# Kernel optimization log

Measured on AMD Instinct MI355X. Metric: run time of the kernel, lower is better.

The kernel has to match this reference:

```python
import jax, jax.numpy as jnp
import numpy as np

S, D_MODEL, D_RNN = 256, 512, 512  # module's broadcasting requires d_rnn == d_model


def setup_inputs() -> dict:
    key = jax.random.key(0)
    k1, k2, k3, k4 = jax.random.split(key, 4)
    x = jax.random.normal(k1, (S, D_MODEL), dtype=jnp.float32)
    state = jnp.zeros((D_RNN, D_MODEL), dtype=jnp.float32)
    # equinox nn.Linear default init: U[-1/sqrt(in), 1/sqrt(in)] for weight and bias
    lim = 1.0 / np.sqrt(D_MODEL)
    W1 = jax.random.uniform(k2, (2 * D_RNN, D_MODEL), minval=-lim, maxval=lim, dtype=jnp.float32)
    b1 = jax.random.uniform(k3, (2 * D_RNN,), minval=-lim, maxval=lim, dtype=jnp.float32)
    # Lambda init exactly as in source: inv_sigmoid(p) = log(1/(1-p)), bounds ** (1/8)
    inv_sig = lambda p: np.log(1.0 / (1.0 - p))
    lower = float(np.power(inv_sig(0.9), 1.0 / 8.0))
    upper = float(np.power(inv_sig(0.999), 1.0 / 8.0))
    Lambda = jax.random.uniform(k4, (D_MODEL,), minval=lower, maxval=upper, dtype=jnp.float32)
    return {"x": x, "state": state, "W1": W1, "b1": b1, "Lambda": Lambda}


def reference(x, state, W1, b1, Lambda):
    # lin1 applied per timestep: (S, d_model) @ (d_model, 2*d_rnn)
    z = jax.nn.sigmoid(x @ W1.T + b1)              # (S, 2*d_rnn)
    inp, rec = jnp.split(z, 2, axis=-1)            # each (S, d_rnn)
    # recurrence gate a_t in (0,1): exp(-8 * softplus(Lambda) * rec)
    a = jnp.exp(-8.0 * jax.nn.softplus(Lambda)[None, :] * rec)  # (S, d_rnn)
    # gated input: outer product per step -> (S, d_rnn, d_model)
    gated_x = jnp.einsum('is,is,id->isd', jnp.sqrt(1.0 - a * a), inp, x)

    def step(h, xs):
        g, at = xs
        h = at[:, None] * h + g                    # (d_rnn, d_model)
        return h, h

    state, y = jax.lax.scan(step, state, (gated_x, a))
    return (y, state)
```

## Files before the change

### kernel.cpp

```cpp
#include <hip/hip_runtime.h>
#include <hip/hip_bf16.h>

#define S_LEN 256
#define DM    512
#define DR    512

typedef float f4 __attribute__((ext_vector_type(4)));
typedef float f2 __attribute__((ext_vector_type(2)));


__global__ __launch_bounds__(256) void k_transpose_x(const float* __restrict__ x,
                                                     float* __restrict__ xT) {
    __shared__ float tile[32][33];
    const int k0 = blockIdx.x * 32;
    const int t0 = blockIdx.y * 32;
    const int lx = threadIdx.x & 31;
    const int ly = threadIdx.x >> 5;
#pragma unroll
    for (int i = 0; i < 32; i += 8)
        tile[ly + i][lx] = x[(t0 + ly + i) * DM + k0 + lx];
    __syncthreads();
#pragma unroll
    for (int i = 0; i < 32; i += 8)
        xT[(k0 + ly + i) * S_LEN + t0 + lx] = tile[lx][ly + i];
}

__global__ __launch_bounds__(256) void k_gemm_act(const float* __restrict__ xT,
                                                  const float* __restrict__ W1,
                                                  const float* __restrict__ b1,
                                                  const float* __restrict__ Lam,
                                                  f2* __restrict__ acT) {
    const int g  = blockIdx.x;
    const int t  = threadIdx.x;
    const int r0 = 2 * g;

    float acc0 = 0.f, acc1 = 0.f, acc2 = 0.f, acc3 = 0.f;
    const float* __restrict__ xb = xT + t;
    const float* __restrict__ w0 = W1 + (r0)       * DM;
    const float* __restrict__ w1 = W1 + (r0 + 1)   * DM;
    const float* __restrict__ w2 = W1 + (512 + r0) * DM;
    const float* __restrict__ w3 = W1 + (513 + r0) * DM;

#pragma unroll 8
    for (int k = 0; k < DM; ++k) {
        const float xv = xb[k * S_LEN];
        acc0 = fmaf(xv, w0[k], acc0);
        acc1 = fmaf(xv, w1[k], acc1);
        acc2 = fmaf(xv, w2[k], acc2);
        acc3 = fmaf(xv, w3[k], acc3);
    }

#pragma unroll
    for (int j = 0; j < 2; ++j) {
        const float pre_i = (j ? acc1 : acc0) + b1[r0 + j];
        const float pre_r = (j ? acc3 : acc2) + b1[512 + r0 + j];
        const float inp = 1.f / (1.f + expf(-pre_i));
        const float rec = 1.f / (1.f + expf(-pre_r));
        const float sp  = log1pf(expf(Lam[r0 + j]));
        const float a   = expf(-8.f * sp * rec);
        const float c   = sqrtf(fmaxf(1.f - a * a, 0.f)) * inp;
        f2 ac; ac.x = a; ac.y = c;
        acT[(r0 + j) * S_LEN + t] = ac;
    }
}

__global__ __launch_bounds__(256) void k_rec(const float* __restrict__ x,
                                             const float* __restrict__ state0,
                                             const f2* __restrict__ acT,
                                             f4* __restrict__ out4) {
    const int bx   = blockIdx.x;
    const int sp   = (bx & 7) * 32 + (bx >> 3);
    const int tid  = threadIdx.x;
    const int half = tid >> 7;
    const int s    = sp * 2 + half;
    const int dq   = tid & 127;

    __shared__ f2 ac_l[2][S_LEN];
    f2* lf = &ac_l[0][0];
    lf[tid]       = acT[sp * 2 * S_LEN + tid];
    lf[tid + 256] = acT[sp * 2 * S_LEN + tid + 256];
    __syncthreads();

    const f4* __restrict__ st4 = reinterpret_cast<const f4*>(state0);
    f4 h = st4[s * 128 + dq];

    const f4* __restrict__ x4 = reinterpret_cast<const f4*>(x);
    f4 xv = x4[dq];

#pragma unroll 4
    for (int t = 0; t < S_LEN; ++t) {
        f4 xn;
        if (t + 1 < S_LEN) xn = x4[(t + 1) * 128 + dq];
        else xn = (f4)0.f;

        const f2 ac = ac_l[half][t];
        const float at = ac.x, ct = ac.y;
        h.x = fmaf(at, h.x, ct * xv.x);
        h.y = fmaf(at, h.y, ct * xv.y);
        h.z = fmaf(at, h.z, ct * xv.z);
        h.w = fmaf(at, h.w, ct * xv.w);

        __builtin_nontemporal_store(h, &out4[(t * DR + s) * 128 + dq]);
        xv = xn;
    }
    out4[(S_LEN * DR) * 128 + s * 128 + dq] = h;
}

extern "C" void kernel_launch(void* const* d_in, const int* in_sizes, int n_in,
                              void* d_out, int out_size, void* d_ws, size_t ws_size,
                              hipStream_t stream) {
    const float* x      = (const float*)d_in[0];
    const float* state0 = (const float*)d_in[1];
    const float* W1     = (const float*)d_in[2];
    const float* b1     = (const float*)d_in[3];
    const float* Lam    = (const float*)d_in[4];

    float* ws  = (float*)d_ws;
    float* xT  = ws;
    f2*    acT = (f2*)(ws + 131072);

    f4* out4 = (f4*)d_out;

    k_transpose_x<<<dim3(16, 8), 256, 0, stream>>>(x, xT);
    k_gemm_act<<<dim3(256), 256, 0, stream>>>(xT, W1, b1, Lam, acT);
    k_rec<<<dim3(256), 256, 0, stream>>>(x, state0, acT, out4);
}
```

Before: 74.43 us.

## Fuse transpose, gate GEMM and recurrence into a single kernel

Merges the three kernels into one. Each block now computes the gate coefficients for its two state rows directly into shared memory, reading x row-wise with float4 loads instead of through a transposed copy, and then runs the recurrence. This removes two launches, the transpose pass and the global round trip of the coefficients. In exchange, each thread reads a whole 2KB row of x with strided per-thread access, which may coalesce poorly.

```diff
diff --git a/kernel.cpp b/kernel.cpp
--- a/kernel.cpp
+++ b/kernel.cpp
@@ -8,84 +8,71 @@
 typedef float f4 __attribute__((ext_vector_type(4)));
 typedef float f2 __attribute__((ext_vector_type(2)));
 
+__global__ __launch_bounds__(256) void k_fused(const float* __restrict__ x,
+                                               const float* __restrict__ state0,
+                                               const float* __restrict__ W1,
+                                               const float* __restrict__ b1,
+                                               const float* __restrict__ Lam,
+                                               f4* __restrict__ out4) {
+    const int bx  = blockIdx.x;
+    const int sp  = (bx & 7) * 32 + (bx >> 3);
+    const int tid = threadIdx.x;
+    const int s0  = sp * 2;
+    const int s1  = sp * 2 + 1;
 
-__global__ __launch_bounds__(256) void k_transpose_x(const float* __restrict__ x,
-                                                     float* __restrict__ xT) {
-    __shared__ float tile[32][33];
-    const int k0 = blockIdx.x * 32;
-    const int t0 = blockIdx.y * 32;
-    const int lx = threadIdx.x & 31;
-    const int ly = threadIdx.x >> 5;
-#pragma unroll
-    for (int i = 0; i < 32; i += 8)
-        tile[ly + i][lx] = x[(t0 + ly + i) * DM + k0 + lx];
-    __syncthreads();
-#pragma unroll
-    for (int i = 0; i < 32; i += 8)
-        xT[(k0 + ly + i) * S_LEN + t0 + lx] = tile[lx][ly + i];
-}
+    __shared__ f2 ac_l[2][S_LEN];
 
-__global__ __launch_bounds__(256) void k_gemm_act(const float* __restrict__ xT,
-                                                  const float* __restrict__ W1,
-                                                  const float* __restrict__ b1,
-                                                  const float* __restrict__ Lam,
-                                                  f2* __restrict__ acT) {
-    const int g  = blockIdx.x;
-    const int t  = threadIdx.x;
-    const int r0 = 2 * g;
+    {
+        const f4* __restrict__ xr  = reinterpret_cast<const f4*>(x) + tid * (DM / 4);
+        const f4* __restrict__ wi0 = reinterpret_cast<const f4*>(W1 + s0 * DM);
+        const f4* __restrict__ wi1 = reinterpret_cast<const f4*>(W1 + s1 * DM);
+        const f4* __restrict__ wr0 = reinterpret_cast<const f4*>(W1 + (DR + s0) * DM);
+        const f4* __restrict__ wr1 = reinterpret_cast<const f4*>(W1 + (DR + s1) * DM);
 
-    float acc0 = 0.f, acc1 = 0.f, acc2 = 0.f, acc3 = 0.f;
-    const float* __restrict__ xb = xT + t;
-    const float* __restrict__ w0 = W1 + (r0)       * DM;
-    const float* __restrict__ w1 = W1 + (r0 + 1)   * DM;
-    const float* __restrict__ w2 = W1 + (512 + r0) * DM;
-    const float* __restrict__ w3 = W1 + (513 + r0) * DM;
+        float ai0 = 0.f, ai1 = 0.f, ar0 = 0.f, ar1 = 0.f;
 
 #pragma unroll 8
-    for (int k = 0; k < DM; ++k) {
-        const float xv = xb[k * S_LEN];
-        acc0 = fmaf(xv, w0[k], acc0);
-        acc1 = fmaf(xv, w1[k], acc1);
-        acc2 = fmaf(xv, w2[k], acc2);
-        acc3 = fmaf(xv, w3[k], acc3);
+        for (int j = 0; j < DM / 4; ++j) {
+            const f4 xv = xr[j];
+            const f4 a = wi0[j];
+            const f4 b = wi1[j];
+            const f4 c = wr0[j];
+            const f4 d = wr1[j];
+            ai0 = fmaf(xv.x, a.x, ai0); ai0 = fmaf(xv.y, a.y, ai0);
+            ai0 = fmaf(xv.z, a.z, ai0); ai0 = fmaf(xv.w, a.w, ai0);
+            ai1 = fmaf(xv.x, b.x, ai1); ai1 = fmaf(xv.y, b.y, ai1);
+            ai1 = fmaf(xv.z, b.z, ai1); ai1 = fmaf(xv.w, b.w, ai1);
+            ar0 = fmaf(xv.x, c.x, ar0); ar0 = fmaf(xv.y, c.y, ar0);
+            ar0 = fmaf(xv.z, c.z, ar0); ar0 = fmaf(xv.w, c.w, ar0);
+            ar1 = fmaf(xv.x, d.x, ar1); ar1 = fmaf(xv.y, d.y, ar1);
+            ar1 = fmaf(xv.z, d.z, ar1); ar1 = fmaf(xv.w, d.w, ar1);
+        }
+
+#pragma unroll
+        for (int j = 0; j < 2; ++j) {
+            const float pre_i = (j ? ai1 : ai0) + b1[(j ? s1 : s0)];
+            const float pre_r = (j ? ar1 : ar0) + b1[DR + (j ? s1 : s0)];
+            const float inp = 1.f / (1.f + expf(-pre_i));
+            const float rec = 1.f / (1.f + expf(-pre_r));
+            const float sof = log1pf(expf(Lam[(j ? s1 : s0)]));
+            const float a   = expf(-8.f * sof * rec);
+            const float c   = sqrtf(fmaxf(1.f - a * a, 0.f)) * inp;
+            f2 ac; ac.x = a; ac.y = c;
+            ac_l[j][tid] = ac;
+        }
     }
 
-#pragma unroll
-    for (int j = 0; j < 2; ++j) {
-        const float pre_i = (j ? acc1 : acc0) + b1[r0 + j];
-        const float pre_r = (j ? acc3 : acc2) + b1[512 + r0 + j];
-        const float inp = 1.f / (1.f + expf(-pre_i));
-        const float rec = 1.f / (1.f + expf(-pre_r));
-        const float sp  = log1pf(expf(Lam[r0 + j]));
-        const float a   = expf(-8.f * sp * rec);
-        const float c   = sqrtf(fmaxf(1.f - a * a, 0.f)) * inp;
-        f2 ac; ac.x = a; ac.y = c;
-        acT[(r0 + j) * S_LEN + t] = ac;
-    }
-}
-
-__global__ __launch_bounds__(256) void k_rec(const float* __restrict__ x,
-                                             const float* __restrict__ state0,
-                                             const f2* __restrict__ acT,
-                                             f4* __restrict__ out4) {
-    const int bx   = blockIdx.x;
-    const int sp   = (bx & 7) * 32 + (bx >> 3);
-    const int tid  = threadIdx.x;
     const int half = tid >> 7;
     const int s    = sp * 2 + half;
     const int dq   = tid & 127;
-
-    __shared__ f2 ac_l[2][S_LEN];
-    f2* lf = &ac_l[0][0];
-    lf[tid]       = acT[sp * 2 * S_LEN + tid];
-    lf[tid + 256] = acT[sp * 2 * S_LEN + tid + 256];
-    __syncthreads();
 
     const f4* __restrict__ st4 = reinterpret_cast<const f4*>(state0);
     f4 h = st4[s * 128 + dq];
 
     const f4* __restrict__ x4 = reinterpret_cast<const f4*>(x);
     f4 xv = x4[dq];
+
+    __syncthreads();
 
 #pragma unroll 4
     for (int t = 0; t < S_LEN; ++t) {
@@ -115,13 +102,7 @@
     const float* b1     = (const float*)d_in[3];
     const float* Lam    = (const float*)d_in[4];
 
-    float* ws  = (float*)d_ws;
-    float* xT  = ws;
-    f2*    acT = (f2*)(ws + 131072);
-
     f4* out4 = (f4*)d_out;
 
-    k_transpose_x<<<dim3(16, 8), 256, 0, stream>>>(x, xT);
-    k_gemm_act<<<dim3(256), 256, 0, stream>>>(xT, W1, b1, Lam, acT);
-    k_rec<<<dim3(256), 256, 0, stream>>>(x, state0, acT, out4);
+    k_fused<<<dim3(256), 256, 0, stream>>>(x, state0, W1, b1, Lam, out4);
 }
```

Result: faster. 69.49 us (-6.6%).
